# Performance work log

Hardware: AMD Instinct MI355X
Metric: run time of the kernel (lower is better)

## Reference

```python
import jax, jax.numpy as jnp
import numpy as np

B = 2
H, W = 128, 128           # branch-0 map_size (target of all scatters)
N0 = 16384                # original grid points = H*W
IN_CH = [64, 128, 256, 512]
NS = [16384, 4096, 1024, 256]
OUT_C = 256
BN_EPS = 1e-5


def setup_inputs() -> dict:
    key = jax.random.key(0)
    ks = jax.random.split(key, 16)
    inp = {}
    for j, (c, n) in enumerate(zip(IN_CH, NS)):
        inp[f"x{j}"] = jax.random.normal(ks[4 * j], (B, n, c), jnp.float32)
        # grid_sample-style coords in [-1, 1]
        inp[f"loc{j}"] = jax.random.uniform(ks[4 * j + 1], (B, N0, 2), jnp.float32) * 2.0 - 1.0
        inp[f"idx{j}"] = jax.random.randint(ks[4 * j + 2], (B, N0), 0, n, dtype=jnp.int32)
        fan_out = 3 * 3 * OUT_C
        inp[f"w{j}"] = jax.random.normal(ks[4 * j + 3], (OUT_C, c, 3, 3), jnp.float32) * np.sqrt(2.0 / fan_out)
        inp[f"gamma{j}"] = jnp.ones((OUT_C,), jnp.float32)
        inp[f"beta{j}"] = jnp.zeros((OUT_C,), jnp.float32)
    return inp


def token2map(x, loc_orig, idx_agg):
    """Scatter-average token features x [B,N,C] onto a dense [B,C,H,W] map.
    Each of N0 original points carries the feature of its token (idx_agg) and
    lands in the grid cell given by loc_orig; cells average their points."""
    Bb, N, C = x.shape
    n0 = loc_orig.shape[1]
    loc = (jnp.clip(loc_orig, -1.0, 1.0) + 1.0) * 0.5
    ix = jnp.clip(jnp.round(loc[..., 0] * (W - 1)).astype(jnp.int32), 0, W - 1)
    iy = jnp.clip(jnp.round(loc[..., 1] * (H - 1)).astype(jnp.int32), 0, H - 1)
    cell = (ix + iy * W + jnp.arange(Bb, dtype=jnp.int32)[:, None] * (H * W)).reshape(-1)  # [B*N0]
    feat = jnp.take_along_axis(x, idx_agg[..., None], axis=1).reshape(Bb * n0, C)  # [B*N0, C]
    ones = jnp.ones((Bb * n0,), x.dtype)
    cnt = jax.ops.segment_sum(ones, cell, num_segments=Bb * H * W) + 1e-6  # points per cell
    val = (1.0 / cnt)[cell]  # per-point normalized weight
    out = jax.ops.segment_sum(feat * val[:, None], cell, num_segments=Bb * H * W)
    return out.reshape(Bb, H, W, C).transpose(0, 3, 1, 2)  # NCHW


def conv_bn(x, w, gamma, beta):
    # 3x3 stride-2 conv (bias=False) + BatchNorm2d (training mode: batch stats, biased var)
    y = jax.lax.conv_general_dilated(x, w, (2, 2), [(1, 1), (1, 1)],
                                     dimension_numbers=('NCHW', 'OIHW', 'NCHW'))
    mean = y.mean(axis=(0, 2, 3))
    var = y.var(axis=(0, 2, 3))
    y = (y - mean[None, :, None, None]) * jax.lax.rsqrt(var + BN_EPS)[None, :, None, None]
    return y * gamma[None, :, None, None] + beta[None, :, None, None]


def reference(x0, x1, x2, x3, loc0, loc1, loc2, loc3, idx0, idx1, idx2, idx3,
              w0, w1, w2, w3, gamma0, gamma1, gamma2, gamma3,
              beta0, beta1, beta2, beta3):
    xs = [x0, x1, x2, x3]
    locs = [loc0, loc1, loc2, loc3]
    idxs = [idx0, idx1, idx2, idx3]
    ws = [w0, w1, w2, w3]
    gs = [gamma0, gamma1, gamma2, gamma3]
    bs = [beta0, beta1, beta2, beta3]
    out_map = 0.0
    for j in range(4):  # fixed small loop over branches (structurally distinct C_j)
        m = token2map(xs[j], locs[j], idxs[j])
        out_map = out_map + conv_bn(m, ws[j], gs[j], bs[j])
    return out_map  # [B, 256, 64, 64]
```

## Files before the change

### kernel.cpp

```cpp
#include <hip/hip_runtime.h>

#define B 2
#define N0 16384
#define HW 16384
#define PADW 130
#define OUTC 256
#define M_ROWS 8192
#define MAXP 32

typedef short s16x8 __attribute__((ext_vector_type(8)));
typedef float f32x4 __attribute__((ext_vector_type(4)));

__device__ __forceinline__ unsigned short f2bf(float f) {
    union { float f; unsigned int u; } v; v.f = f;
    unsigned int u = v.u;
    return (unsigned short)((u + 0x7fffu + ((u >> 16) & 1u)) >> 16);
}
__device__ __forceinline__ float bf2f(unsigned short h) {
    union { unsigned int u; float f; } v; v.u = ((unsigned int)h) << 16;
    return v.f;
}

__device__ __forceinline__ void gl_lds16(const void* g, void* l) {
    __builtin_amdgcn_global_load_lds(
        (const __attribute__((address_space(1))) unsigned int*)g,
        (__attribute__((address_space(3))) unsigned int*)l, 16, 0, 0);
}

__device__ __forceinline__ void cell_of(const float* __restrict__ loc, int r, int& ix, int& iy) {
    float lx = loc[r * 2 + 0];
    float ly = loc[r * 2 + 1];
    lx = fminf(fmaxf(lx, -1.f), 1.f);
    ly = fminf(fmaxf(ly, -1.f), 1.f);
    ix = min(max((int)rintf(((lx + 1.f) * 0.5f) * 127.f), 0), 127);
    iy = min(max((int)rintf(((ly + 1.f) * 0.5f) * 127.f), 0), 127);
}

__global__ void fill_k(const float* __restrict__ l0, const float* __restrict__ l1,
                       const float* __restrict__ l2, const float* __restrict__ l3,
                       const int* __restrict__ i0, const int* __restrict__ i1,
                       const int* __restrict__ i2, const int* __restrict__ i3,
                       int* __restrict__ cnt32, unsigned short* __restrict__ list) {
    int p = blockIdx.x * 256 + threadIdx.x;
    int j = p >> 15, r = p & 32767;
    const float* loc = j == 0 ? l0 : j == 1 ? l1 : j == 2 ? l2 : l3;
    const int* idx = j == 0 ? i0 : j == 1 ? i1 : j == 2 ? i2 : i3;
    int ix, iy;
    cell_of(loc, r, ix, iy);
    int cidx = (((j << 1) + (r >> 14)) << 14) + iy * 128 + ix;
    int pos = atomicAdd(&cnt32[cidx], 1);
    if (pos < MAXP) list[cidx * MAXP + pos] = (unsigned short)idx[r];
}

__global__ void gather_k(const float* __restrict__ x0, const float* __restrict__ x1,
                         const float* __restrict__ x2, const float* __restrict__ x3,
                         const int* __restrict__ cnt32, const unsigned short* __restrict__ list,
                         unsigned short* __restrict__ mapB) {
    int W = (blockIdx.x * 256 + threadIdx.x) >> 6;
    if (W >= 63375) return;
    int lane = threadIdx.x & 63;
    int j, base;
    if (W < 4225) { j = 0; base = 0; }
    else if (W < 12675) { j = 1; base = 4225; }
    else if (W < 29575) { j = 2; base = 12675; }
    else { j = 3; base = 29575; }
    const float* x = j == 0 ? x0 : j == 1 ? x1 : j == 2 ? x2 : x3;
    const int C = 64 << j;
    const int ntok = 16384 >> (2 * j);
    int u = W - base;
    int cellLocal = (u << (3 - j)) + (lane >> (3 + j));
    int sub = lane & ((8 << j) - 1);
    int ch0 = sub * 8;
    int b = cellLocal / 16900;
    int cc = cellLocal - b * 16900;
    int py = cc / 130, px = cc - py * 130;
    unsigned short* dst = mapB + (size_t)33800 * (C - 64) +
                          ((size_t)cellLocal * C) + ch0;
    float a0 = 0.f, a1 = 0.f, a2 = 0.f, a3 = 0.f, a4 = 0.f, a5 = 0.f, a6 = 0.f, a7 = 0.f;
    if (py >= 1 && py <= 128 && px >= 1 && px <= 128) {
        int cidx = (((j << 1) + b) << 14) + (py - 1) * 128 + (px - 1);
        int n = cnt32[cidx];
        float inv = 1.0f / ((float)n + 1e-6f);
        int nn = min(n, MAXP);
        const unsigned short* lst = list + (size_t)cidx * MAXP;
        for (int p = 0; p < nn; p++) {
            int tok = lst[p];
            const float* xr = x + ((size_t)b * ntok + tok) * C + ch0;
            float4 v0 = *(const float4*)xr;
            float4 v1 = *(const float4*)(xr + 4);
            a0 += v0.x; a1 += v0.y; a2 += v0.z; a3 += v0.w;
            a4 += v1.x; a5 += v1.y; a6 += v1.z; a7 += v1.w;
        }
        a0 *= inv; a1 *= inv; a2 *= inv; a3 *= inv;
        a4 *= inv; a5 *= inv; a6 *= inv; a7 *= inv;
    }
    uint4 o;
    o.x = (unsigned int)f2bf(a0) | ((unsigned int)f2bf(a1) << 16);
    o.y = (unsigned int)f2bf(a2) | ((unsigned int)f2bf(a3) << 16);
    o.z = (unsigned int)f2bf(a4) | ((unsigned int)f2bf(a5) << 16);
    o.w = (unsigned int)f2bf(a6) | ((unsigned int)f2bf(a7) << 16);
    *(uint4*)dst = o;
}

__global__ void wprep_all(const float* __restrict__ w0, const float* __restrict__ w1,
                          const float* __restrict__ w2, const float* __restrict__ w3,
                          unsigned short* __restrict__ wt) {
    int i = blockIdx.x * 256 + threadIdx.x;
    if (i >= 2211840) return;
    int j, local;
    if (i < 147456) { j = 0; local = i; }
    else if (i < 442368) { j = 1; local = i - 147456; }
    else if (i < 1032192) { j = 2; local = i - 442368; }
    else { j = 3; local = i - 1032192; }
    const float* w = j == 0 ? w0 : j == 1 ? w1 : j == 2 ? w2 : w3;
    int lc = 6 + j, C = 1 << lc;
    int ci = local & (C - 1);
    int rest = local >> lc;
    int seg = rest % 9, co = rest / 9;
    int kh = seg / 3, kw = seg % 3;
    wt[(size_t)2304 * (C - 64) + local] = f2bf(w[(((co * C) + ci) * 3 + kh) * 3 + kw]);
}

__global__ __launch_bounds__(256, 4) void conv_mfma(const unsigned short* __restrict__ mapB,
                                                    const unsigned short* __restrict__ wt,
                                                    unsigned short* __restrict__ P,
                                                    float* __restrict__ partial) {
    __shared__ unsigned short As[2][128][32];
    __shared__ unsigned short Bs[2][128][32];
    __shared__ float red_s[4][64], red_ss[4][64];
    const int t = threadIdx.x;
    const int lane = t & 63;
    const int w = t >> 6;
    const int wm = w >> 1, wn = w & 1;
    const int z = blockIdx.z;
    const int j = (z < 4) ? 3 : (z < 6) ? 2 : (z == 6) ? 1 : 0;
    const int lc = 6 + j;
    const int C = 1 << lc;
    const int K = 9 * C;
    const int s0 = (z < 4) ? z * 36 : (z == 5 ? 36 : 0);
    const int s1 = s0 + (j == 0 ? 18 : 36);
    const unsigned short* mapBj = mapB + (size_t)33800 * (C - 64);
    const unsigned short* wtj = wt + (size_t)2304 * (C - 64);
    unsigned short* Pz = P + (size_t)z * M_ROWS * OUTC;
    const int mt = blockIdx.x, nt = blockIdx.y;

    const int lr = lane >> 2, lq = lane & 3;
    const unsigned short* pA[2];
    const unsigned short* pB[2];
#pragma unroll
    for (int i = 0; i < 2; i++) {
        int r = w * 32 + i * 16 + lr;
        int s = mt * 128 + r;
        int b = s >> 12, rem = s & 4095, oh = rem >> 6, ow = rem & 63;
        pA[i] = mapBj + (size_t)((b * PADW + 2 * oh) * PADW + 2 * ow) * C + lq * 8;
        pB[i] = wtj + (size_t)(nt * 128 + r) * K + lq * 8;
    }

    int k0 = s0 << 5;
    int seg0 = k0 >> lc;
    int ci0 = k0 & (C - 1);
    int kh = seg0 / 3, kw = seg0 - 3 * kh;
    int offA = (kh * PADW + kw) * C + ci0;
    int offB = k0;

    gl_lds16(pA[0] + offA, &As[0][w * 32][0]);
    gl_lds16(pA[1] + offA, &As[0][w * 32 + 16][0]);
    gl_lds16(pB[0] + offB, &Bs[0][w * 32][0]);
    gl_lds16(pB[1] + offB, &Bs[0][w * 32 + 16][0]);

    f32x4 acc[4][4];
#pragma unroll
    for (int mi = 0; mi < 4; mi++)
#pragma unroll
        for (int ni = 0; ni < 4; ni++) acc[mi][ni] = (f32x4){0.f, 0.f, 0.f, 0.f};

    const int r16 = lane & 15, kg = lane >> 4;
    int buf = 0;
    for (int s = s0; s < s1; s++) {
        ci0 += 32; offA += 32; offB += 32;
        if (ci0 == C) {
            ci0 = 0; kw++;
            if (kw == 3) { kw = 0; offA += (PADW - 3) * C; }
        }
        __syncthreads();
        if (s + 1 < s1) {
            int nb = buf ^ 1;
            gl_lds16(pA[0] + offA, &As[nb][w * 32][0]);
            gl_lds16(pA[1] + offA, &As[nb][w * 32 + 16][0]);
            gl_lds16(pB[0] + offB, &Bs[nb][w * 32][0]);
            gl_lds16(pB[1] + offB, &Bs[nb][w * 32 + 16][0]);
        }
        s16x8 a0 = *(const s16x8*)&As[buf][wm * 64 + 0 * 16 + r16][kg * 8];
        s16x8 a1 = *(const s16x8*)&As[buf][wm * 64 + 1 * 16 + r16][kg * 8];
        s16x8 a2 = *(const s16x8*)&As[buf][wm * 64 + 2 * 16 + r16][kg * 8];
        s16x8 a3 = *(const s16x8*)&As[buf][wm * 64 + 3 * 16 + r16][kg * 8];
        s16x8 b0 = *(const s16x8*)&Bs[buf][wn * 64 + 0 * 16 + r16][kg * 8];
        s16x8 b1 = *(const s16x8*)&Bs[buf][wn * 64 + 1 * 16 + r16][kg * 8];
        s16x8 b2 = *(const s16x8*)&Bs[buf][wn * 64 + 2 * 16 + r16][kg * 8];
        s16x8 b3 = *(const s16x8*)&Bs[buf][wn * 64 + 3 * 16 + r16][kg * 8];
        acc[0][0] = __builtin_amdgcn_mfma_f32_16x16x32_bf16(a0, b0, acc[0][0], 0, 0, 0);
        acc[0][1] = __builtin_amdgcn_mfma_f32_16x16x32_bf16(a0, b1, acc[0][1], 0, 0, 0);
        acc[0][2] = __builtin_amdgcn_mfma_f32_16x16x32_bf16(a0, b2, acc[0][2], 0, 0, 0);
        acc[0][3] = __builtin_amdgcn_mfma_f32_16x16x32_bf16(a0, b3, acc[0][3], 0, 0, 0);
        acc[1][0] = __builtin_amdgcn_mfma_f32_16x16x32_bf16(a1, b0, acc[1][0], 0, 0, 0);
        acc[1][1] = __builtin_amdgcn_mfma_f32_16x16x32_bf16(a1, b1, acc[1][1], 0, 0, 0);
        acc[1][2] = __builtin_amdgcn_mfma_f32_16x16x32_bf16(a1, b2, acc[1][2], 0, 0, 0);
        acc[1][3] = __builtin_amdgcn_mfma_f32_16x16x32_bf16(a1, b3, acc[1][3], 0, 0, 0);
        acc[2][0] = __builtin_amdgcn_mfma_f32_16x16x32_bf16(a2, b0, acc[2][0], 0, 0, 0);
        acc[2][1] = __builtin_amdgcn_mfma_f32_16x16x32_bf16(a2, b1, acc[2][1], 0, 0, 0);
        acc[2][2] = __builtin_amdgcn_mfma_f32_16x16x32_bf16(a2, b2, acc[2][2], 0, 0, 0);
        acc[2][3] = __builtin_amdgcn_mfma_f32_16x16x32_bf16(a2, b3, acc[2][3], 0, 0, 0);
        acc[3][0] = __builtin_amdgcn_mfma_f32_16x16x32_bf16(a3, b0, acc[3][0], 0, 0, 0);
        acc[3][1] = __builtin_amdgcn_mfma_f32_16x16x32_bf16(a3, b1, acc[3][1], 0, 0, 0);
        acc[3][2] = __builtin_amdgcn_mfma_f32_16x16x32_bf16(a3, b2, acc[3][2], 0, 0, 0);
        acc[3][3] = __builtin_amdgcn_mfma_f32_16x16x32_bf16(a3, b3, acc[3][3], 0, 0, 0);
        buf ^= 1;
    }

    const int rg = lane >> 4, c16 = lane & 15;
#pragma unroll
    for (int mi = 0; mi < 4; mi++)
#pragma unroll
        for (int ni = 0; ni < 4; ni++)
#pragma unroll
            for (int reg = 0; reg < 4; reg++) {
                int row = mt * 128 + wm * 64 + mi * 16 + rg * 4 + reg;
                int col = nt * 128 + wn * 64 + ni * 16 + c16;
                Pz[(size_t)row * OUTC + col] = f2bf(acc[mi][ni][reg]);
            }

#pragma unroll
    for (int ni = 0; ni < 4; ni++) {
        float s = 0.f, ss = 0.f;
#pragma unroll
        for (int mi = 0; mi < 4; mi++)
#pragma unroll
            for (int reg = 0; reg < 4; reg++) {
                float v = acc[mi][ni][reg];
                s += v;
                ss += v * v;
            }
        s += __shfl_xor(s, 16, 64);
        ss += __shfl_xor(ss, 16, 64);
        s += __shfl_xor(s, 32, 64);
        ss += __shfl_xor(ss, 32, 64);
        if (rg == 0) {
            red_s[w][ni * 16 + c16] = s;
            red_ss[w][ni * 16 + c16] = ss;
        }
    }
    __syncthreads();
    if (t < 128) {
        int col = t;
        int cwn = col >> 6, rem = col & 63;
        float s = red_s[cwn][rem] + red_s[cwn + 2][rem];
        float ss = red_ss[cwn][rem] + red_ss[cwn + 2][rem];
        float* pb = partial + ((size_t)((z * 2 + nt) * 64 + mt)) * 256;
        pb[col] = s;
        pb[128 + col] = ss;
    }
}

__global__ void stats2_k(const float* __restrict__ partial,
                         const float* __restrict__ g0, const float* __restrict__ g1,
                         const float* __restrict__ g2, const float* __restrict__ g3,
                         const float* __restrict__ b0, const float* __restrict__ b1,
                         const float* __restrict__ b2, const float* __restrict__ b3,
                         float* __restrict__ ssb) {
    int j = blockIdx.x, c = threadIdx.x;
    const float* gamma = j == 0 ? g0 : j == 1 ? g1 : j == 2 ? g2 : g3;
    const float* beta = j == 0 ? b0 : j == 1 ? b1 : j == 2 ? b2 : b3;
    int zs = j == 3 ? 0 : j == 2 ? 4 : j == 1 ? 6 : 7;
    int nz = j == 3 ? 4 : j == 2 ? 2 : 1;
    int nt = c >> 7, col = c & 127;
    float s = 0.f, ss = 0.f;
    for (int z = zs; z < zs + nz; z++)
        for (int mt = 0; mt < 64; mt++) {
            const float* pb = partial + ((size_t)((z * 2 + nt) * 64 + mt)) * 256;
            s += pb[col];
            ss += pb[128 + col];
        }
    float mean = s * (1.f / 8192.f);
    float var = ss * (1.f / 8192.f) - mean * mean;
    float rs = rsqrtf(var + 1e-5f);
    float sc = gamma[c] * rs;
    ssb[j * 512 + c] = sc;
    ssb[j * 512 + OUTC + c] = beta[c] - mean * sc;
}

__global__ void out_k(const unsigned short* __restrict__ P, const float* __restrict__ ssb,
                      float* __restrict__ out) {
    __shared__ float tile[64][132];
    int oh = blockIdx.x, ct = blockIdx.y, b = blockIdx.z;
    int t = threadIdx.x;
    int cg = t & 31, rt = t >> 5;
    int c0 = ct * 128 + cg * 4;
    float sc[4][4], sh[4];
#pragma unroll
    for (int k = 0; k < 4; k++) {
        float shk = 0.f;
#pragma unroll
        for (int jj = 0; jj < 4; jj++) {
            sc[jj][k] = ssb[jj * 512 + c0 + k];
            shk += ssb[jj * 512 + OUTC + c0 + k];
        }
        sh[k] = shk;
    }
#pragma unroll
    for (int it = 0; it < 8; it++) {
        int ow = rt * 8 + it;
        size_t row = (size_t)b * 4096 + oh * 64 + ow;
        const unsigned short* p = P + row * OUTC + c0;
        float a3k[4], a2k[4], a1k[4], a0k[4];
#pragma unroll
        for (int k = 0; k < 4; k++) { a3k[k] = a2k[k] = a1k[k] = a0k[k] = 0.f; }
#pragma unroll
        for (int zz = 0; zz < 8; zz++) {
            ushort4 u = *(const ushort4*)(p + (size_t)zz * M_ROWS * OUTC);
            float* a = zz < 4 ? a3k : zz < 6 ? a2k : (zz == 6 ? a1k : a0k);
            a[0] += bf2f(u.x);
            a[1] += bf2f(u.y);
            a[2] += bf2f(u.z);
            a[3] += bf2f(u.w);
        }
#pragma unroll
        for (int k = 0; k < 4; k++)
            tile[ow][cg * 4 + k] = sh[k] + a3k[k] * sc[3][k] + a2k[k] * sc[2][k] +
                                   a1k[k] * sc[1][k] + a0k[k] * sc[0][k];
    }
    __syncthreads();
    int owq = t & 15, cp = t >> 4;
#pragma unroll
    for (int pass = 0; pass < 8; pass++) {
        int c = pass * 16 + cp;
        float4 v;
        v.x = tile[owq * 4 + 0][c];
        v.y = tile[owq * 4 + 1][c];
        v.z = tile[owq * 4 + 2][c];
        v.w = tile[owq * 4 + 3][c];
        *(float4*)(out + (((size_t)b * OUTC + ct * 128 + c) * 64 + oh) * 64 + owq * 4) = v;
    }
}

extern "C" void kernel_launch(void* const* d_in, const int* in_sizes, int n_in,
                              void* d_out, int out_size, void* d_ws, size_t ws_size,
                              hipStream_t stream) {
    char* ws = (char*)d_ws;
    size_t off = 0;
    auto alloc = [&](size_t bytes) {
        void* p = ws + off;
        off = (off + bytes + 255) & ~(size_t)255;
        return p;
    };
    unsigned short* P = (unsigned short*)alloc((size_t)8 * M_ROWS * OUTC * 2);
    unsigned short* wt = (unsigned short*)alloc((size_t)2304 * 960 * 2);
    unsigned short* mapB = (unsigned short*)alloc((size_t)33800 * 960 * 2);
    int* cnt32 = (int*)alloc((size_t)4 * 2 * HW * 4);
    unsigned short* list = (unsigned short*)alloc((size_t)4 * 2 * HW * MAXP * 2);
    float* partial = (float*)alloc((size_t)1024 * 256 * 4);
    float* ssb = (float*)alloc((size_t)4 * 512 * 4);

    hipMemsetAsync(cnt32, 0, (size_t)4 * 2 * HW * 4, stream);

    fill_k<<<512, 256, 0, stream>>>(
        (const float*)d_in[1], (const float*)d_in[7], (const float*)d_in[13],
        (const float*)d_in[19],
        (const int*)d_in[2], (const int*)d_in[8], (const int*)d_in[14],
        (const int*)d_in[20], cnt32, list);
    wprep_all<<<8640, 256, 0, stream>>>(
        (const float*)d_in[3], (const float*)d_in[9], (const float*)d_in[15],
        (const float*)d_in[21], wt);
    gather_k<<<15844, 256, 0, stream>>>(
        (const float*)d_in[0], (const float*)d_in[6], (const float*)d_in[12],
        (const float*)d_in[18], cnt32, list, mapB);
    conv_mfma<<<dim3(64, 2, 8), 256, 0, stream>>>(mapB, wt, P, partial);
    stats2_k<<<4, 256, 0, stream>>>(partial,
        (const float*)d_in[4], (const float*)d_in[10], (const float*)d_in[16],
        (const float*)d_in[22],
        (const float*)d_in[5], (const float*)d_in[11], (const float*)d_in[17],
        (const float*)d_in[23], ssb);
    out_k<<<dim3(64, 2, 2), 256, 0, stream>>>(P, ssb, (float*)d_out);
}
```

Baseline: 215.7 us.

## Apply conv weights per token before scatter for deep branches

For branches 2 and 3, which have few tokens but many channels, the code now multiplies each token's features by all nine 3x3 weight slices up front in a small GEMM (T = x·W). The conv output is then assembled by gathering T rows through the cell lists with count weighting, instead of first building dense 128x128 maps and convolving them. Branches 0 and 1 keep the conv path. Weight prep, the bf16 conversion of x and gathering now share one kernel. BN statistics are accumulated with atomics, and the separate stats kernel is folded into out_k. This removes most of the conv FLOPs and map traffic for the large-channel branches, at the cost of an irregular gather in asm_k and extra T buffers.

```diff
diff --git a/kernel.cpp b/kernel.cpp
--- a/kernel.cpp
+++ b/kernel.cpp
@@ -1,7 +1,6 @@
 #include <hip/hip_runtime.h>
 
 #define B 2
-#define N0 16384
 #define HW 16384
 #define PADW 130
 #define OUTC 256
@@ -52,19 +51,51 @@
     if (pos < MAXP) list[cidx * MAXP + pos] = (unsigned short)idx[r];
 }
 
-__global__ void gather_k(const float* __restrict__ x0, const float* __restrict__ x1,
-                         const float* __restrict__ x2, const float* __restrict__ x3,
-                         const int* __restrict__ cnt32, const unsigned short* __restrict__ list,
-                         unsigned short* __restrict__ mapB) {
+__global__ void prep2_k(const float* __restrict__ x0, const float* __restrict__ x1,
+                        const int* __restrict__ cnt32, const unsigned short* __restrict__ list,
+                        unsigned short* __restrict__ mapB01,
+                        const float* __restrict__ w0, const float* __restrict__ w1,
+                        const float* __restrict__ w2, const float* __restrict__ w3,
+                        unsigned short* __restrict__ wt01,
+                        unsigned short* __restrict__ wtg2, unsigned short* __restrict__ wtg3,
+                        const float* __restrict__ x2, const float* __restrict__ x3,
+                        unsigned short* __restrict__ xb2, unsigned short* __restrict__ xb3) {
+    if (blockIdx.x >= 3169) {
+        int e = (blockIdx.x - 3169) * 256 + threadIdx.x;
+        if (e < 442368) {
+            int j = e < 147456 ? 0 : 1;
+            int local = j ? e - 147456 : e;
+            const float* w = j ? w1 : w0;
+            int lc = 6 + j, C = 1 << lc;
+            int ci = local & (C - 1);
+            int rest = local >> lc;
+            int seg = rest % 9, co = rest / 9;
+            int kh = seg / 3, kw = seg % 3;
+            wt01[e] = f2bf(w[(((co * C) + ci) * 3 + kh) * 3 + kw]);
+        } else if (e < 2211840) {
+            int j = e < 1032192 ? 2 : 3;
+            int local = j == 2 ? e - 442368 : e - 1032192;
+            const float* w = j == 2 ? w2 : w3;
+            int lc = 6 + j, C = 1 << lc;
+            int ci = local & (C - 1);
+            int nrow = local >> lc;
+            int kk = nrow >> 8, co = nrow & 255;
+            int kh = kk / 3, kw = kk % 3;
+            unsigned short* dst = j == 2 ? wtg2 : wtg3;
+            dst[local] = f2bf(w[(((co * C) + ci) * 3 + kh) * 3 + kw]);
+        } else if (e < 2736128) {
+            xb2[e - 2211840] = f2bf(x2[e - 2211840]);
+        } else {
+            xb3[e - 2736128] = f2bf(x3[e - 2736128]);
+        }
+        return;
+    }
     int W = (blockIdx.x * 256 + threadIdx.x) >> 6;
-    if (W >= 63375) return;
+    if (W >= 12675) return;
     int lane = threadIdx.x & 63;
-    int j, base;
-    if (W < 4225) { j = 0; base = 0; }
-    else if (W < 12675) { j = 1; base = 4225; }
-    else if (W < 29575) { j = 2; base = 12675; }
-    else { j = 3; base = 29575; }
-    const float* x = j == 0 ? x0 : j == 1 ? x1 : j == 2 ? x2 : x3;
+    int j = (W < 4225) ? 0 : 1;
+    int base = j ? 4225 : 0;
+    const float* x = j ? x1 : x0;
     const int C = 64 << j;
     const int ntok = 16384 >> (2 * j);
     int u = W - base;
@@ -74,8 +105,7 @@
     int b = cellLocal / 16900;
     int cc = cellLocal - b * 16900;
     int py = cc / 130, px = cc - py * 130;
-    unsigned short* dst = mapB + (size_t)33800 * (C - 64) +
-                          ((size_t)cellLocal * C) + ch0;
+    unsigned short* dst = mapB01 + (size_t)33800 * (C - 64) + (size_t)cellLocal * C + ch0;
     float a0 = 0.f, a1 = 0.f, a2 = 0.f, a3 = 0.f, a4 = 0.f, a5 = 0.f, a6 = 0.f, a7 = 0.f;
     if (py >= 1 && py <= 128 && px >= 1 && px <= 128) {
         int cidx = (((j << 1) + b) << 14) + (py - 1) * 128 + (px - 1);
@@ -102,29 +132,16 @@
     *(uint4*)dst = o;
 }
 
-__global__ void wprep_all(const float* __restrict__ w0, const float* __restrict__ w1,
-                          const float* __restrict__ w2, const float* __restrict__ w3,
-                          unsigned short* __restrict__ wt) {
-    int i = blockIdx.x * 256 + threadIdx.x;
-    if (i >= 2211840) return;
-    int j, local;
-    if (i < 147456) { j = 0; local = i; }
-    else if (i < 442368) { j = 1; local = i - 147456; }
-    else if (i < 1032192) { j = 2; local = i - 442368; }
-    else { j = 3; local = i - 1032192; }
-    const float* w = j == 0 ? w0 : j == 1 ? w1 : j == 2 ? w2 : w3;
-    int lc = 6 + j, C = 1 << lc;
-    int ci = local & (C - 1);
-    int rest = local >> lc;
-    int seg = rest % 9, co = rest / 9;
-    int kh = seg / 3, kw = seg % 3;
-    wt[(size_t)2304 * (C - 64) + local] = f2bf(w[(((co * C) + ci) * 3 + kh) * 3 + kw]);
-}
-
-__global__ __launch_bounds__(256, 4) void conv_mfma(const unsigned short* __restrict__ mapB,
-                                                    const unsigned short* __restrict__ wt,
-                                                    unsigned short* __restrict__ P,
-                                                    float* __restrict__ partial) {
+__global__ __launch_bounds__(256) void mm_k(const unsigned short* __restrict__ mapB01,
+                                            const unsigned short* __restrict__ wt01,
+                                            const unsigned short* __restrict__ xb2,
+                                            const unsigned short* __restrict__ xb3,
+                                            const unsigned short* __restrict__ wtg2,
+                                            const unsigned short* __restrict__ wtg3,
+                                            unsigned short* __restrict__ T2,
+                                            unsigned short* __restrict__ T3,
+                                            unsigned short* __restrict__ ybr,
+                                            float* __restrict__ branchAcc) {
     __shared__ unsigned short As[2][128][32];
     __shared__ unsigned short Bs[2][128][32];
     __shared__ float red_s[4][64], red_ss[4][64];
@@ -132,17 +149,34 @@
     const int lane = t & 63;
     const int w = t >> 6;
     const int wm = w >> 1, wn = w & 1;
-    const int z = blockIdx.z;
-    const int j = (z < 4) ? 3 : (z < 6) ? 2 : (z == 6) ? 1 : 0;
-    const int lc = 6 + j;
-    const int C = 1 << lc;
-    const int K = 9 * C;
-    const int s0 = (z < 4) ? z * 36 : (z == 5 ? 36 : 0);
-    const int s1 = s0 + (j == 0 ? 18 : 36);
-    const unsigned short* mapBj = mapB + (size_t)33800 * (C - 64);
-    const unsigned short* wtj = wt + (size_t)2304 * (C - 64);
-    unsigned short* Pz = P + (size_t)z * M_ROWS * OUTC;
-    const int mt = blockIdx.x, nt = blockIdx.y;
+    const int bx = blockIdx.x;
+
+    bool isconv;
+    int j, mt, nt, K, steps, C, bgem = 0;
+    const unsigned short *Abase, *Bbase;
+    if (bx < 128) {
+        isconv = true; j = 1; mt = bx & 63; nt = (bx >> 6) & 1;
+        C = 128; K = 9 * C; steps = 36;
+        Abase = mapB01 + (size_t)33800 * 64;
+        Bbase = wt01 + (size_t)2304 * 64;
+    } else if (bx < 200) {
+        isconv = false; j = 3; int r = bx - 128;
+        bgem = r / 36; r %= 36; mt = r / 18; nt = r % 18;
+        C = 512; K = C; steps = 16;
+        Abase = xb3 + (size_t)bgem * 256 * 512;
+        Bbase = wtg3;
+    } else if (bx < 488) {
+        isconv = false; j = 2; int r = bx - 200;
+        bgem = r / 144; r %= 144; mt = r / 18; nt = r % 18;
+        C = 256; K = C; steps = 8;
+        Abase = xb2 + (size_t)bgem * 1024 * 256;
+        Bbase = wtg2;
+    } else {
+        isconv = true; j = 0; int r = bx - 488; mt = r & 63; nt = (r >> 6) & 1;
+        C = 64; K = 9 * C; steps = 18;
+        Abase = mapB01;
+        Bbase = wt01;
+    }
 
     const int lr = lane >> 2, lq = lane & 3;
     const unsigned short* pA[2];
@@ -150,23 +184,21 @@
 #pragma unroll
     for (int i = 0; i < 2; i++) {
         int r = w * 32 + i * 16 + lr;
-        int s = mt * 128 + r;
-        int b = s >> 12, rem = s & 4095, oh = rem >> 6, ow = rem & 63;
-        pA[i] = mapBj + (size_t)((b * PADW + 2 * oh) * PADW + 2 * ow) * C + lq * 8;
-        pB[i] = wtj + (size_t)(nt * 128 + r) * K + lq * 8;
-    }
-
-    int k0 = s0 << 5;
-    int seg0 = k0 >> lc;
-    int ci0 = k0 & (C - 1);
-    int kh = seg0 / 3, kw = seg0 - 3 * kh;
-    int offA = (kh * PADW + kw) * C + ci0;
-    int offB = k0;
-
-    gl_lds16(pA[0] + offA, &As[0][w * 32][0]);
-    gl_lds16(pA[1] + offA, &As[0][w * 32 + 16][0]);
-    gl_lds16(pB[0] + offB, &Bs[0][w * 32][0]);
-    gl_lds16(pB[1] + offB, &Bs[0][w * 32 + 16][0]);
+        if (isconv) {
+            int s = mt * 128 + r;
+            int bb = s >> 12, rem = s & 4095, oh = rem >> 6, ow = rem & 63;
+            pA[i] = Abase + (size_t)((bb * PADW + 2 * oh) * PADW + 2 * ow) * C + lq * 8;
+        } else {
+            pA[i] = Abase + (size_t)(mt * 128 + r) * K + lq * 8;
+        }
+        pB[i] = Bbase + (size_t)(nt * 128 + r) * K + lq * 8;
+    }
+
+    int ci0 = 0, kwv = 0, offA = 0, offB = 0;
+    gl_lds16(pA[0], &As[0][w * 32][0]);
+    gl_lds16(pA[1], &As[0][w * 32 + 16][0]);
+    gl_lds16(pB[0], &Bs[0][w * 32][0]);
+    gl_lds16(pB[1], &Bs[0][w * 32 + 16][0]);
 
     f32x4 acc[4][4];
 #pragma unroll
@@ -176,14 +208,19 @@
 
     const int r16 = lane & 15, kg = lane >> 4;
     int buf = 0;
-    for (int s = s0; s < s1; s++) {
-        ci0 += 32; offA += 32; offB += 32;
-        if (ci0 == C) {
-            ci0 = 0; kw++;
-            if (kw == 3) { kw = 0; offA += (PADW - 3) * C; }
+    for (int s = 0; s < steps; s++) {
+        offB += 32;
+        if (isconv) {
+            ci0 += 32; offA += 32;
+            if (ci0 == C) {
+                ci0 = 0; kwv++;
+                if (kwv == 3) { kwv = 0; offA += (PADW - 3) * C; }
+            }
+        } else {
+            offA += 32;
         }
         __syncthreads();
-        if (s + 1 < s1) {
+        if (s + 1 < steps) {
             int nb = buf ^ 1;
             gl_lds16(pA[0] + offA, &As[nb][w * 32][0]);
             gl_lds16(pA[1] + offA, &As[nb][w * 32 + 16][0]);
@@ -218,77 +255,140 @@
     }
 
     const int rg = lane >> 4, c16 = lane & 15;
-#pragma unroll
-    for (int mi = 0; mi < 4; mi++)
-#pragma unroll
-        for (int ni = 0; ni < 4; ni++)
-#pragma unroll
-            for (int reg = 0; reg < 4; reg++) {
-                int row = mt * 128 + wm * 64 + mi * 16 + rg * 4 + reg;
-                int col = nt * 128 + wn * 64 + ni * 16 + c16;
-                Pz[(size_t)row * OUTC + col] = f2bf(acc[mi][ni][reg]);
+    if (!isconv) {
+        unsigned short* T = (j == 3) ? T3 + (size_t)bgem * 256 * 2304
+                                     : T2 + (size_t)bgem * 1024 * 2304;
+#pragma unroll
+        for (int mi = 0; mi < 4; mi++)
+#pragma unroll
+            for (int ni = 0; ni < 4; ni++)
+#pragma unroll
+                for (int reg = 0; reg < 4; reg++) {
+                    int row = mt * 128 + wm * 64 + mi * 16 + rg * 4 + reg;
+                    int col = nt * 128 + wn * 64 + ni * 16 + c16;
+                    T[(size_t)row * 2304 + col] = f2bf(acc[mi][ni][reg]);
+                }
+    } else {
+#pragma unroll
+        for (int mi = 0; mi < 4; mi++)
+#pragma unroll
+            for (int ni = 0; ni < 4; ni++)
+#pragma unroll
+                for (int reg = 0; reg < 4; reg++) {
+                    int row = mt * 128 + wm * 64 + mi * 16 + rg * 4 + reg;
+                    int col = nt * 128 + wn * 64 + ni * 16 + c16;
+                    ybr[((size_t)j * M_ROWS + row) * OUTC + col] = f2bf(acc[mi][ni][reg]);
+                }
+#pragma unroll
+        for (int ni = 0; ni < 4; ni++) {
+            float s = 0.f, ss = 0.f;
+#pragma unroll
+            for (int mi = 0; mi < 4; mi++)
+#pragma unroll
+                for (int reg = 0; reg < 4; reg++) {
+                    float v = acc[mi][ni][reg];
+                    s += v;
+                    ss += v * v;
+                }
+            s += __shfl_xor(s, 16, 64);
+            ss += __shfl_xor(ss, 16, 64);
+            s += __shfl_xor(s, 32, 64);
+            ss += __shfl_xor(ss, 32, 64);
+            if (rg == 0) {
+                red_s[w][ni * 16 + c16] = s;
+                red_ss[w][ni * 16 + c16] = ss;
             }
-
-#pragma unroll
-    for (int ni = 0; ni < 4; ni++) {
-        float s = 0.f, ss = 0.f;
-#pragma unroll
-        for (int mi = 0; mi < 4; mi++)
-#pragma unroll
-            for (int reg = 0; reg < 4; reg++) {
-                float v = acc[mi][ni][reg];
-                s += v;
-                ss += v * v;
+        }
+        __syncthreads();
+        if (t < 128) {
+            int col = t;
+            int cwn = col >> 6, rem = col & 63;
+            float s = red_s[cwn][rem] + red_s[cwn + 2][rem];
+            float ss = red_ss[cwn][rem] + red_ss[cwn + 2][rem];
+            int ch = nt * 128 + col;
+            atomicAdd(&branchAcc[j * 512 + ch], s);
+            atomicAdd(&branchAcc[j * 512 + 256 + ch], ss);
+        }
+    }
+}
+
+__global__ __launch_bounds__(256) void asm_k(const int* __restrict__ cnt32,
+                                             const unsigned short* __restrict__ list,
+                                             const unsigned short* __restrict__ T2,
+                                             const unsigned short* __restrict__ T3,
+                                             unsigned short* __restrict__ ybr,
+                                             float* __restrict__ branchAcc) {
+    __shared__ float red[4][256];
+    int t = threadIdx.x, lane = t & 63, w = t >> 6;
+    int bi = blockIdx.x;
+    int ch4 = lane << 2;
+    float sreg[2][4], ssreg[2][4];
+#pragma unroll
+    for (int jj = 0; jj < 2; jj++)
+#pragma unroll
+        for (int k = 0; k < 4; k++) { sreg[jj][k] = 0.f; ssreg[jj][k] = 0.f; }
+
+    for (int it = 0; it < 8; it++) {
+        int srow = bi * 32 + w * 8 + it;
+        int b = srow >> 12, rem = srow & 4095, oh = rem >> 6, ow = rem & 63;
+#pragma unroll
+        for (int jj = 0; jj < 2; jj++) {
+            int j = 2 + jj;
+            int nj = jj ? 256 : 1024;
+            const unsigned short* T = jj ? T3 : T2;
+            float a0 = 0.f, a1 = 0.f, a2 = 0.f, a3 = 0.f;
+            for (int kh = 0; kh < 3; kh++) {
+                int iy = 2 * oh + kh - 1;
+                if ((unsigned)iy >= 128u) continue;
+                for (int kw = 0; kw < 3; kw++) {
+                    int ix = 2 * ow + kw - 1;
+                    if ((unsigned)ix >= 128u) continue;
+                    int cidx = (((j << 1) + b) << 14) + iy * 128 + ix;
+                    int n = cnt32[cidx];
+                    if (n == 0) continue;
+                    float wc = 1.0f / ((float)n + 1e-6f);
+                    int nn = min(n, MAXP);
+                    const unsigned short* lst = list + (size_t)cidx * MAXP;
+                    float t0 = 0.f, t1 = 0.f, t2 = 0.f, t3 = 0.f;
+                    for (int p = 0; p < nn; p++) {
+                        int tok = lst[p];
+                        const unsigned short* Tp =
+                            T + ((size_t)(b * nj + tok) * 2304 + (kh * 3 + kw) * 256 + ch4);
+                        ushort4 u = *(const ushort4*)Tp;
+                        t0 += bf2f(u.x);
+                        t1 += bf2f(u.y);
+                        t2 += bf2f(u.z);
+                        t3 += bf2f(u.w);
+                    }
+                    a0 += wc * t0; a1 += wc * t1; a2 += wc * t2; a3 += wc * t3;
+                }
             }
-        s += __shfl_xor(s, 16, 64);
-        ss += __shfl_xor(ss, 16, 64);
-        s += __shfl_xor(s, 32, 64);
-        ss += __shfl_xor(ss, 32, 64);
-        if (rg == 0) {
-            red_s[w][ni * 16 + c16] = s;
-            red_ss[w][ni * 16 + c16] = ss;
-        }
-    }
-    __syncthreads();
-    if (t < 128) {
-        int col = t;
-        int cwn = col >> 6, rem = col & 63;
-        float s = red_s[cwn][rem] + red_s[cwn + 2][rem];
-        float ss = red_ss[cwn][rem] + red_ss[cwn + 2][rem];
-        float* pb = partial + ((size_t)((z * 2 + nt) * 64 + mt)) * 256;
-        pb[col] = s;
-        pb[128 + col] = ss;
-    }
-}
-
-__global__ void stats2_k(const float* __restrict__ partial,
-                         const float* __restrict__ g0, const float* __restrict__ g1,
-                         const float* __restrict__ g2, const float* __restrict__ g3,
-                         const float* __restrict__ b0, const float* __restrict__ b1,
-                         const float* __restrict__ b2, const float* __restrict__ b3,
-                         float* __restrict__ ssb) {
-    int j = blockIdx.x, c = threadIdx.x;
-    const float* gamma = j == 0 ? g0 : j == 1 ? g1 : j == 2 ? g2 : g3;
-    const float* beta = j == 0 ? b0 : j == 1 ? b1 : j == 2 ? b2 : b3;
-    int zs = j == 3 ? 0 : j == 2 ? 4 : j == 1 ? 6 : 7;
-    int nz = j == 3 ? 4 : j == 2 ? 2 : 1;
-    int nt = c >> 7, col = c & 127;
-    float s = 0.f, ss = 0.f;
-    for (int z = zs; z < zs + nz; z++)
-        for (int mt = 0; mt < 64; mt++) {
-            const float* pb = partial + ((size_t)((z * 2 + nt) * 64 + mt)) * 256;
-            s += pb[col];
-            ss += pb[128 + col];
-        }
-    float mean = s * (1.f / 8192.f);
-    float var = ss * (1.f / 8192.f) - mean * mean;
-    float rs = rsqrtf(var + 1e-5f);
-    float sc = gamma[c] * rs;
-    ssb[j * 512 + c] = sc;
-    ssb[j * 512 + OUTC + c] = beta[c] - mean * sc;
-}
-
-__global__ void out_k(const unsigned short* __restrict__ P, const float* __restrict__ ssb,
+            ushort4 o;
+            o.x = f2bf(a0); o.y = f2bf(a1); o.z = f2bf(a2); o.w = f2bf(a3);
+            *(ushort4*)(ybr + ((size_t)j * M_ROWS + srow) * OUTC + ch4) = o;
+            sreg[jj][0] += a0; sreg[jj][1] += a1; sreg[jj][2] += a2; sreg[jj][3] += a3;
+            ssreg[jj][0] += a0 * a0; ssreg[jj][1] += a1 * a1;
+            ssreg[jj][2] += a2 * a2; ssreg[jj][3] += a3 * a3;
+        }
+    }
+    for (int pass = 0; pass < 4; pass++) {
+        const float* src = (pass == 0) ? sreg[0] : (pass == 1) ? ssreg[0]
+                            : (pass == 2) ? sreg[1] : ssreg[1];
+#pragma unroll
+        for (int k = 0; k < 4; k++) red[w][ch4 + k] = src[k];
+        __syncthreads();
+        float S = red[0][t] + red[1][t] + red[2][t] + red[3][t];
+        __syncthreads();
+        int jb = (pass >> 1) ? 3 : 2;
+        atomicAdd(&branchAcc[jb * 512 + (pass & 1) * 256 + t], S);
+    }
+}
+
+__global__ void out_k(const unsigned short* __restrict__ ybr, const float* __restrict__ branchAcc,
+                      const float* __restrict__ g0, const float* __restrict__ g1,
+                      const float* __restrict__ g2, const float* __restrict__ g3,
+                      const float* __restrict__ b0, const float* __restrict__ b1,
+                      const float* __restrict__ b2, const float* __restrict__ b3,
                       float* __restrict__ out) {
     __shared__ float tile[64][132];
     int oh = blockIdx.x, ct = blockIdx.y, b = blockIdx.z;
@@ -298,11 +398,20 @@
     float sc[4][4], sh[4];
 #pragma unroll
     for (int k = 0; k < 4; k++) {
+        int c = c0 + k;
         float shk = 0.f;
 #pragma unroll
         for (int jj = 0; jj < 4; jj++) {
-            sc[jj][k] = ssb[jj * 512 + c0 + k];
-            shk += ssb[jj * 512 + OUTC + c0 + k];
+            const float* gamma = jj == 0 ? g0 : jj == 1 ? g1 : jj == 2 ? g2 : g3;
+            const float* beta = jj == 0 ? b0 : jj == 1 ? b1 : jj == 2 ? b2 : b3;
+            float sum = branchAcc[jj * 512 + c];
+            float sumsq = branchAcc[jj * 512 + 256 + c];
+            float mean = sum * (1.f / 8192.f);
+            float var = sumsq * (1.f / 8192.f) - mean * mean;
+            float rs = rsqrtf(var + 1e-5f);
+            float scv = gamma[c] * rs;
+            sc[jj][k] = scv;
+            shk += beta[c] - mean * scv;
         }
         sh[k] = shk;
     }
@@ -310,23 +419,20 @@
     for (int it = 0; it < 8; it++) {
         int ow = rt * 8 + it;
         size_t row = (size_t)b * 4096 + oh * 64 + ow;
-        const unsigned short* p = P + row * OUTC + c0;
-        float a3k[4], a2k[4], a1k[4], a0k[4];
-#pragma unroll
-        for (int k = 0; k < 4; k++) { a3k[k] = a2k[k] = a1k[k] = a0k[k] = 0.f; }
-#pragma unroll
-        for (int zz = 0; zz < 8; zz++) {
-            ushort4 u = *(const ushort4*)(p + (size_t)zz * M_ROWS * OUTC);
-            float* a = zz < 4 ? a3k : zz < 6 ? a2k : (zz == 6 ? a1k : a0k);
-            a[0] += bf2f(u.x);
-            a[1] += bf2f(u.y);
-            a[2] += bf2f(u.z);
-            a[3] += bf2f(u.w);
-        }
-#pragma unroll
-        for (int k = 0; k < 4; k++)
-            tile[ow][cg * 4 + k] = sh[k] + a3k[k] * sc[3][k] + a2k[k] * sc[2][k] +
-                                   a1k[k] * sc[1][k] + a0k[k] * sc[0][k];
+        const unsigned short* p = ybr + row * OUTC + c0;
+        float acc[4];
+#pragma unroll
+        for (int k = 0; k < 4; k++) acc[k] = sh[k];
+#pragma unroll
+        for (int jj = 0; jj < 4; jj++) {
+            ushort4 u = *(const ushort4*)(p + (size_t)jj * M_ROWS * OUTC);
+            acc[0] += bf2f(u.x) * sc[jj][0];
+            acc[1] += bf2f(u.y) * sc[jj][1];
+            acc[2] += bf2f(u.z) * sc[jj][2];
+            acc[3] += bf2f(u.w) * sc[jj][3];
+        }
+#pragma unroll
+        for (int k = 0; k < 4; k++) tile[ow][cg * 4 + k] = acc[k];
     }
     __syncthreads();
     int owq = t & 15, cp = t >> 4;
@@ -352,32 +458,36 @@
         off = (off + bytes + 255) & ~(size_t)255;
         return p;
     };
-    unsigned short* P = (unsigned short*)alloc((size_t)8 * M_ROWS * OUTC * 2);
-    unsigned short* wt = (unsigned short*)alloc((size_t)2304 * 960 * 2);
-    unsigned short* mapB = (unsigned short*)alloc((size_t)33800 * 960 * 2);
+    unsigned short* ybr = (unsigned short*)alloc((size_t)4 * M_ROWS * OUTC * 2);
+    unsigned short* wt01 = (unsigned short*)alloc((size_t)442368 * 2);
+    unsigned short* wtg2 = (unsigned short*)alloc((size_t)589824 * 2);
+    unsigned short* wtg3 = (unsigned short*)alloc((size_t)1179648 * 2);
+    unsigned short* xb2 = (unsigned short*)alloc((size_t)524288 * 2);
+    unsigned short* xb3 = (unsigned short*)alloc((size_t)262144 * 2);
+    unsigned short* T2 = (unsigned short*)alloc((size_t)2 * 1024 * 2304 * 2);
+    unsigned short* T3 = (unsigned short*)alloc((size_t)2 * 256 * 2304 * 2);
+    unsigned short* mapB01 = (unsigned short*)alloc((size_t)33800 * 192 * 2);
     int* cnt32 = (int*)alloc((size_t)4 * 2 * HW * 4);
+    float* branchAcc = (float*)alloc((size_t)4 * 512 * 4);
     unsigned short* list = (unsigned short*)alloc((size_t)4 * 2 * HW * MAXP * 2);
-    float* partial = (float*)alloc((size_t)1024 * 256 * 4);
-    float* ssb = (float*)alloc((size_t)4 * 512 * 4);
-
-    hipMemsetAsync(cnt32, 0, (size_t)4 * 2 * HW * 4, stream);
+
+    hipMemsetAsync(cnt32, 0, (size_t)4 * 2 * HW * 4 + 4 * 512 * 4, stream);
 
     fill_k<<<512, 256, 0, stream>>>(
         (const float*)d_in[1], (const float*)d_in[7], (const float*)d_in[13],
         (const float*)d_in[19],
         (const int*)d_in[2], (const int*)d_in[8], (const int*)d_in[14],
         (const int*)d_in[20], cnt32, list);
-    wprep_all<<<8640, 256, 0, stream>>>(
+    prep2_k<<<3169 + 11712, 256, 0, stream>>>(
+        (const float*)d_in[0], (const float*)d_in[6], cnt32, list, mapB01,
         (const float*)d_in[3], (const float*)d_in[9], (const float*)d_in[15],
-        (const float*)d_in[21], wt);
-    gather_k<<<15844, 256, 0, stream>>>(
-        (const float*)d_in[0], (const float*)d_in[6], (const float*)d_in[12],
-        (const float*)d_in[18], cnt32, list, mapB);
-    conv_mfma<<<dim3(64, 2, 8), 256, 0, stream>>>(mapB, wt, P, partial);
-    stats2_k<<<4, 256, 0, stream>>>(partial,
+        (const float*)d_in[21], wt01, wtg2, wtg3,
+        (const float*)d_in[12], (const float*)d_in[18], xb2, xb3);
+    mm_k<<<616, 256, 0, stream>>>(mapB01, wt01, xb2, xb3, wtg2, wtg3, T2, T3, ybr, branchAcc);
+    asm_k<<<256, 256, 0, stream>>>(cnt32, list, T2, T3, ybr, branchAcc);
+    out_k<<<dim3(64, 2, 2), 256, 0, stream>>>(ybr, branchAcc,
         (const float*)d_in[4], (const float*)d_in[10], (const float*)d_in[16],
         (const float*)d_in[22],
         (const float*)d_in[5], (const float*)d_in[11], (const float*)d_in[17],
-        (const float*)d_in[23], ssb);
-    out_k<<<dim3(64, 2, 2), 256, 0, stream>>>(P, ssb, (float*)d_out);
-}
+        (const float*)d_in[23], (float*)d_out);
+}
```

After: 276.0 us. 27.9% more time.
